# Kernel optimization log

Measured on AMD Instinct MI355X. Metric: run time of the kernel, lower is better.

The kernel has to match this reference:

```python
import math
import jax
import jax.numpy as jnp
import numpy as np

N_QUBITS = 4
N_LAYERS = 2


def _ry(t):
    # t: [] or [B] real angle -> [2,2] or [B,2,2] complex RY matrix
    c, s = jnp.cos(t * 0.5), jnp.sin(t * 0.5)
    return jnp.stack([jnp.stack([c, -s], -1), jnp.stack([s, c], -1)], -2).astype(jnp.complex64)


def _rz(t):
    # t: [] or [B] real angle -> diag(e^{-it/2}, e^{+it/2}) complex RZ matrix
    ph = jnp.exp(-0.5j * t.astype(jnp.complex64))
    z = jnp.zeros_like(ph)
    return jnp.stack([jnp.stack([ph, z], -1), jnp.stack([z, jnp.conj(ph)], -1)], -2)


def _apply_1q(psi, U, w):
    # psi: [B,2,2,2,2]; U: [2,2] (shared) or [B,2,2] (per-sample); wire w
    psi = jnp.moveaxis(psi, 1 + w, -1)
    if U.ndim == 3:
        out = jnp.einsum('bij,bpqrj->bpqri', U, psi)
    else:
        out = jnp.einsum('ij,bpqrj->bpqri', U, psi)
    return jnp.moveaxis(out, -1, 1 + w)


def _cnot(psi, c):
    # CNOT with control wire c, target wire c+1 (matches qml.CNOT([w, w+1]))
    a0 = jax.lax.index_in_dim(psi, 0, axis=1 + c, keepdims=False)
    a1 = jax.lax.index_in_dim(psi, 1, axis=1 + c, keepdims=False)
    a1 = jnp.flip(a1, axis=1 + c)
    return jnp.stack([a0, a1], axis=1 + c)


def _circuit(angles, q_weights):
    # angles: [B,4] real; q_weights: [n_layers,4,2]
    B = angles.shape[0]
    psi = jnp.zeros((B, 2, 2, 2, 2), jnp.complex64).at[:, 0, 0, 0, 0].set(1.0)
    for layer in range(N_LAYERS):
        for w in range(N_QUBITS):
            psi = _apply_1q(psi, _ry(angles[:, w]), w)
            psi = _apply_1q(psi, _rz((layer + 1) * angles[:, w]), w)
        for w in range(N_QUBITS):
            psi = _apply_1q(psi, _ry(q_weights[layer, w, 0]), w)
            psi = _apply_1q(psi, _rz(q_weights[layer, w, 1]), w)
        for w in range(N_QUBITS - 1):
            psi = _cnot(psi, w)
    p = psi.real ** 2 + psi.imag ** 2  # [B,2,2,2,2] probabilities
    zs = []
    for w in range(N_QUBITS):
        axes = tuple(a for a in range(1, 1 + N_QUBITS) if a != 1 + w)
        s = jnp.sum(p, axis=axes)  # [B,2]
        zs.append(s[:, 0] - s[:, 1])
    return jnp.stack(zs, -1).astype(jnp.float32)  # [B,4] <Z_w> expvals


def setup_inputs() -> dict:
    key = jax.random.key(0)
    ks = jax.random.split(key, 8)
    B, D = 131072, 256
    return {
        'x': jax.random.normal(ks[0], (B, D), jnp.float32),
        'w_proj': jax.random.normal(ks[1], (4, D), jnp.float32) / np.float32(np.sqrt(D)),
        'b_proj': jnp.zeros((4,), jnp.float32),
        'q_weights': 0.01 * jax.random.normal(ks[2], (2, 4, 2), jnp.float32),
        'w_h': jax.random.normal(ks[3], (16, 4), jnp.float32) * np.float32(0.5),
        'b_h': jnp.zeros((16,), jnp.float32),
        'w_out': jax.random.normal(ks[4], (10, 16), jnp.float32) * np.float32(0.25),
        'b_out': jnp.zeros((10,), jnp.float32),
    }


def reference(x, w_proj, b_proj, q_weights, w_h, b_h, w_out, b_out):
    # input_proj -> tanh * pi -> per-sample quantum circuit -> MLP classifier
    angles = jnp.tanh(x @ w_proj.T + b_proj) * np.float32(math.pi)  # [B,4]
    q = _circuit(angles, q_weights)                                  # [B,4]
    h = jax.nn.relu(q @ w_h.T + b_h)                                 # [B,16]
    return h @ w_out.T + b_out                                       # [B,10]
```

## Files before the change

### kernel.cpp

```cpp
#include <hip/hip_runtime.h>
#include <math.h>

#define D    256
#define BLK  64
#define RPC  8
#define NCH  (BLK/RPC)

struct C2 { float x, y; };

__device__ __forceinline__ float4 shfl_xor4(float4 a, int m) {
  float4 r;
  r.x = __shfl_xor(a.x, m); r.y = __shfl_xor(a.y, m);
  r.z = __shfl_xor(a.z, m); r.w = __shfl_xor(a.w, m);
  return r;
}
__device__ __forceinline__ float4 add4(float4 a, float4 b) {
  return make_float4(a.x+b.x, a.y+b.y, a.z+b.z, a.w+b.w);
}

__device__ __forceinline__ void gate_ry(C2 st[16], const int m, float c, float s) {
#pragma unroll
  for (int i = 0; i < 16; ++i) {
    if (i & m) continue;
    const int i1 = i | m;
    C2 a0 = st[i], a1 = st[i1];
    st[i].x  = c*a0.x - s*a1.x;  st[i].y  = c*a0.y - s*a1.y;
    st[i1].x = s*a0.x + c*a1.x;  st[i1].y = s*a0.y + c*a1.y;
  }
}

__device__ __forceinline__ void gate_rz(C2 st[16], const int m, float c, float s) {
#pragma unroll
  for (int i = 0; i < 16; ++i) {
    C2 a = st[i];
    if (i & m) { st[i].x = a.x*c - a.y*s; st[i].y = a.y*c + a.x*s; }
    else       { st[i].x = a.x*c + a.y*s; st[i].y = a.y*c - a.x*s; }
  }
}

__global__ __launch_bounds__(BLK, 4) void qhead_kernel(
    const float4* __restrict__ x4,
    const float*  __restrict__ w_proj,
    const float*  __restrict__ b_proj,
    const float*  __restrict__ qw,
    const float*  __restrict__ w_h,
    const float*  __restrict__ b_h,
    const float*  __restrict__ w_out,
    const float*  __restrict__ b_out,
    float*        __restrict__ out)
{
  __shared__ float outS[BLK * 11];

  const int tid = threadIdx.x;
  const long s0 = (long)blockIdx.x * BLK;
  const float4* xrow = x4 + s0 * (D / 4);

  float4 wj[4];
#pragma unroll
  for (int j = 0; j < 4; ++j)
    wj[j] = *(const float4*)(w_proj + j * D + 4 * tid);

  float4 v[8];
#pragma unroll
  for (int i = 0; i < 8; ++i) v[i] = xrow[(long)i * (D/4) + tid];

  const int b5 = (tid >> 5) & 1, b4 = (tid >> 4) & 1, b3 = (tid >> 3) & 1;
  const int csel = tid & 7;
  float4 acc = make_float4(0.f, 0.f, 0.f, 0.f);

#pragma unroll 1
  for (int c = 0; c < NCH; ++c) {
    float4 p[8];
#pragma unroll
    for (int i = 0; i < 8; ++i) {
      p[i].x = v[i].x*wj[0].x + v[i].y*wj[0].y + v[i].z*wj[0].z + v[i].w*wj[0].w;
      p[i].y = v[i].x*wj[1].x + v[i].y*wj[1].y + v[i].z*wj[1].z + v[i].w*wj[1].w;
      p[i].z = v[i].x*wj[2].x + v[i].y*wj[2].y + v[i].z*wj[2].z + v[i].w*wj[2].w;
      p[i].w = v[i].x*wj[3].x + v[i].y*wj[3].y + v[i].z*wj[3].z + v[i].w*wj[3].w;
    }
    if (c + 1 < NCH) {
#pragma unroll
      for (int i = 0; i < 8; ++i)
        v[i] = xrow[((long)(c + 1) * RPC + i) * (D/4) + tid];
    }
    float4 q[4];
#pragma unroll
    for (int i = 0; i < 4; ++i) {
      float4 send = b5 ? p[i] : p[i + 4];
      float4 keep = b5 ? p[i + 4] : p[i];
      q[i] = add4(keep, shfl_xor4(send, 32));
    }
    float4 u[2];
#pragma unroll
    for (int i = 0; i < 2; ++i) {
      float4 send = b4 ? u[0] : u[0];
      (void)send;
      float4 s2 = b4 ? q[i] : q[i + 2];
      float4 k2 = b4 ? q[i + 2] : q[i];
      u[i] = add4(k2, shfl_xor4(s2, 16));
    }
    float4 t;
    {
      float4 s3 = b3 ? u[0] : u[1];
      float4 k3 = b3 ? u[1] : u[0];
      t = add4(k3, shfl_xor4(s3, 8));
    }
    t = add4(t, shfl_xor4(t, 4));
    t = add4(t, shfl_xor4(t, 2));
    t = add4(t, shfl_xor4(t, 1));
    if (csel == c) acc = t;
  }

  const float PI_F = 3.14159265358979f;
  float ang[4];
  ang[0] = tanhf(acc.x + b_proj[0]) * PI_F;
  ang[1] = tanhf(acc.y + b_proj[1]) * PI_F;
  ang[2] = tanhf(acc.z + b_proj[2]) * PI_F;
  ang[3] = tanhf(acc.w + b_proj[3]) * PI_F;

  float ch[4], sh[4], cf[4], sf[4];
#pragma unroll
  for (int w = 0; w < 4; ++w) {
    __sincosf(0.5f * ang[w], &sh[w], &ch[w]);
    __sincosf(ang[w], &sf[w], &cf[w]);
  }

  C2 st[16];
#pragma unroll
  for (int i = 0; i < 16; ++i) { st[i].x = 0.f; st[i].y = 0.f; }
  st[0].x = 1.f;

#pragma unroll
  for (int layer = 0; layer < 2; ++layer) {
#pragma unroll
    for (int w = 0; w < 4; ++w) {
      gate_ry(st, 8 >> w, ch[w], sh[w]);
      if (layer == 0) gate_rz(st, 8 >> w, ch[w], sh[w]);
      else            gate_rz(st, 8 >> w, cf[w], sf[w]);
    }
#pragma unroll
    for (int w = 0; w < 4; ++w) {
      float cw, sw, cz, sz;
      __sincosf(0.5f * qw[(layer * 4 + w) * 2 + 0], &sw, &cw);
      __sincosf(0.5f * qw[(layer * 4 + w) * 2 + 1], &sz, &cz);
      gate_ry(st, 8 >> w, cw, sw);
      gate_rz(st, 8 >> w, cz, sz);
    }
#pragma unroll
    for (int w = 0; w < 3; ++w) {
      const int mc = 8 >> w, mt = 4 >> w;
#pragma unroll
      for (int i = 0; i < 16; ++i) {
        if ((i & mc) && !(i & mt)) {
          C2 t2 = st[i]; st[i] = st[i | mt]; st[i | mt] = t2;
        }
      }
    }
  }

  float z[4] = {0.f, 0.f, 0.f, 0.f};
#pragma unroll
  for (int i = 0; i < 16; ++i) {
    const float p = st[i].x * st[i].x + st[i].y * st[i].y;
#pragma unroll
    for (int w = 0; w < 4; ++w) z[w] += (i & (8 >> w)) ? -p : p;
  }

  float outv[10];
  {
    float h[16];
#pragma unroll
    for (int j = 0; j < 16; ++j) {
      float a = b_h[j];
#pragma unroll
      for (int w = 0; w < 4; ++w) a += w_h[j * 4 + w] * z[w];
      h[j] = fmaxf(a, 0.f);
    }
#pragma unroll
    for (int o = 0; o < 10; ++o) {
      float a = b_out[o];
#pragma unroll
      for (int j = 0; j < 16; ++j) a += w_out[o * 16 + j] * h[j];
      outv[o] = a;
    }
  }

  const int smp = 8 * csel + (tid >> 3);
#pragma unroll
  for (int o = 0; o < 10; ++o) outS[smp * 11 + o] = outv[o];
  __syncthreads();
  float* og = out + (long)blockIdx.x * (BLK * 10);
#pragma unroll
  for (int i = 0; i < 10; ++i) {
    const int j = i * BLK + tid;
    og[j] = outS[(j / 10) * 11 + (j % 10)];
  }
}

extern "C" void kernel_launch(void* const* d_in, const int* in_sizes, int n_in,
                              void* d_out, int out_size, void* d_ws, size_t ws_size,
                              hipStream_t stream) {
  const int B = in_sizes[0] / D;
  dim3 grid(B / BLK), block(BLK);
  qhead_kernel<<<grid, block, 0, stream>>>(
      (const float4*)d_in[0],
      (const float*)d_in[1], (const float*)d_in[2], (const float*)d_in[3],
      (const float*)d_in[4], (const float*)d_in[5], (const float*)d_in[6],
      (const float*)d_in[7], (float*)d_out);
}
```

Before: 210.8 us.

## Halve samples per block and double-buffer x row loads

Each block now handles 32 samples instead of 64, so the grid has twice as many blocks. Two register buffers of 8 rows each are kept, so loads for the next two chunks are in flight while the current chunk is reduced. The aim is more memory-level parallelism for what looks like a latency-bound projection. The cost is more registers (launch bounds lowered to 3) and every sample's circuit and MLP now being computed by two threads, which doubles that redundant compute.

```diff
diff --git a/kernel.cpp b/kernel.cpp
--- a/kernel.cpp
+++ b/kernel.cpp
@@ -3,8 +3,9 @@
 
 #define D    256
 #define BLK  64
+#define SPB  32
 #define RPC  8
-#define NCH  (BLK/RPC)
+#define NCH  (SPB/RPC)
 
 struct C2 { float x, y; };
 
@@ -38,7 +39,48 @@
   }
 }
 
-__global__ __launch_bounds__(BLK, 4) void qhead_kernel(
+#define PHASE(V, c)                                                          \
+  {                                                                          \
+    float4 p[8];                                                             \
+    _Pragma("unroll")                                                        \
+    for (int i = 0; i < 8; ++i) {                                            \
+      p[i].x = V[i].x*wj[0].x + V[i].y*wj[0].y + V[i].z*wj[0].z + V[i].w*wj[0].w; \
+      p[i].y = V[i].x*wj[1].x + V[i].y*wj[1].y + V[i].z*wj[1].z + V[i].w*wj[1].w; \
+      p[i].z = V[i].x*wj[2].x + V[i].y*wj[2].y + V[i].z*wj[2].z + V[i].w*wj[2].w; \
+      p[i].w = V[i].x*wj[3].x + V[i].y*wj[3].y + V[i].z*wj[3].z + V[i].w*wj[3].w; \
+    }                                                                        \
+    if ((c) + 2 < NCH) {                                                     \
+      _Pragma("unroll")                                                      \
+      for (int i = 0; i < 8; ++i)                                            \
+        V[i] = xrow[((long)((c) + 2) * RPC + i) * (D/4) + tid];              \
+    }                                                                        \
+    float4 q[4];                                                             \
+    _Pragma("unroll")                                                        \
+    for (int i = 0; i < 4; ++i) {                                            \
+      float4 snd = b5 ? p[i] : p[i + 4];                                     \
+      float4 kp  = b5 ? p[i + 4] : p[i];                                     \
+      q[i] = add4(kp, shfl_xor4(snd, 32));                                   \
+    }                                                                        \
+    float4 u[2];                                                             \
+    _Pragma("unroll")                                                        \
+    for (int i = 0; i < 2; ++i) {                                            \
+      float4 snd = b4 ? q[i] : q[i + 2];                                     \
+      float4 kp  = b4 ? q[i + 2] : q[i];                                     \
+      u[i] = add4(kp, shfl_xor4(snd, 16));                                   \
+    }                                                                        \
+    float4 t;                                                                \
+    {                                                                        \
+      float4 snd = b3 ? u[0] : u[1];                                         \
+      float4 kp  = b3 ? u[1] : u[0];                                         \
+      t = add4(kp, shfl_xor4(snd, 8));                                       \
+    }                                                                        \
+    t = add4(t, shfl_xor4(t, 4));                                            \
+    t = add4(t, shfl_xor4(t, 2));                                            \
+    t = add4(t, shfl_xor4(t, 1));                                            \
+    if (csel == (c)) acc = t;                                                \
+  }
+
+__global__ __launch_bounds__(BLK, 3) void qhead_kernel(
     const float4* __restrict__ x4,
     const float*  __restrict__ w_proj,
     const float*  __restrict__ b_proj,
@@ -49,10 +91,10 @@
     const float*  __restrict__ b_out,
     float*        __restrict__ out)
 {
-  __shared__ float outS[BLK * 11];
+  __shared__ float outS[SPB * 11];
 
   const int tid = threadIdx.x;
-  const long s0 = (long)blockIdx.x * BLK;
+  const long s0 = (long)blockIdx.x * SPB;
   const float4* xrow = x4 + s0 * (D / 4);
 
   float4 wj[4];
@@ -60,55 +102,20 @@
   for (int j = 0; j < 4; ++j)
     wj[j] = *(const float4*)(w_proj + j * D + 4 * tid);
 
-  float4 v[8];
-#pragma unroll
-  for (int i = 0; i < 8; ++i) v[i] = xrow[(long)i * (D/4) + tid];
-
   const int b5 = (tid >> 5) & 1, b4 = (tid >> 4) & 1, b3 = (tid >> 3) & 1;
-  const int csel = tid & 7;
+  const int csel = tid & 3;
   float4 acc = make_float4(0.f, 0.f, 0.f, 0.f);
 
+  float4 vA[8], vB[8];
+#pragma unroll
+  for (int i = 0; i < 8; ++i) vA[i] = xrow[(long)i * (D/4) + tid];
+#pragma unroll
+  for (int i = 0; i < 8; ++i) vB[i] = xrow[(long)(RPC + i) * (D/4) + tid];
+
 #pragma unroll 1
-  for (int c = 0; c < NCH; ++c) {
-    float4 p[8];
-#pragma unroll
-    for (int i = 0; i < 8; ++i) {
-      p[i].x = v[i].x*wj[0].x + v[i].y*wj[0].y + v[i].z*wj[0].z + v[i].w*wj[0].w;
-      p[i].y = v[i].x*wj[1].x + v[i].y*wj[1].y + v[i].z*wj[1].z + v[i].w*wj[1].w;
-      p[i].z = v[i].x*wj[2].x + v[i].y*wj[2].y + v[i].z*wj[2].z + v[i].w*wj[2].w;
-      p[i].w = v[i].x*wj[3].x + v[i].y*wj[3].y + v[i].z*wj[3].z + v[i].w*wj[3].w;
-    }
-    if (c + 1 < NCH) {
-#pragma unroll
-      for (int i = 0; i < 8; ++i)
-        v[i] = xrow[((long)(c + 1) * RPC + i) * (D/4) + tid];
-    }
-    float4 q[4];
-#pragma unroll
-    for (int i = 0; i < 4; ++i) {
-      float4 send = b5 ? p[i] : p[i + 4];
-      float4 keep = b5 ? p[i + 4] : p[i];
-      q[i] = add4(keep, shfl_xor4(send, 32));
-    }
-    float4 u[2];
-#pragma unroll
-    for (int i = 0; i < 2; ++i) {
-      float4 send = b4 ? u[0] : u[0];
-      (void)send;
-      float4 s2 = b4 ? q[i] : q[i + 2];
-      float4 k2 = b4 ? q[i + 2] : q[i];
-      u[i] = add4(k2, shfl_xor4(s2, 16));
-    }
-    float4 t;
-    {
-      float4 s3 = b3 ? u[0] : u[1];
-      float4 k3 = b3 ? u[1] : u[0];
-      t = add4(k3, shfl_xor4(s3, 8));
-    }
-    t = add4(t, shfl_xor4(t, 4));
-    t = add4(t, shfl_xor4(t, 2));
-    t = add4(t, shfl_xor4(t, 1));
-    if (csel == c) acc = t;
+  for (int cc = 0; cc < NCH; cc += 2) {
+    PHASE(vA, cc);
+    PHASE(vB, cc + 1);
   }
 
   const float PI_F = 3.14159265358979f;
@@ -189,9 +196,9 @@
 #pragma unroll
   for (int o = 0; o < 10; ++o) outS[smp * 11 + o] = outv[o];
   __syncthreads();
-  float* og = out + (long)blockIdx.x * (BLK * 10);
-#pragma unroll
-  for (int i = 0; i < 10; ++i) {
+  float* og = out + (long)blockIdx.x * (SPB * 10);
+#pragma unroll
+  for (int i = 0; i < 5; ++i) {
     const int j = i * BLK + tid;
     og[j] = outS[(j / 10) * 11 + (j % 10)];
   }
@@ -201,7 +208,7 @@
                               void* d_out, int out_size, void* d_ws, size_t ws_size,
                               hipStream_t stream) {
   const int B = in_sizes[0] / D;
-  dim3 grid(B / BLK), block(BLK);
+  dim3 grid(B / SPB), block(BLK);
   qhead_kernel<<<grid, block, 0, stream>>>(
       (const float4*)d_in[0],
       (const float*)d_in[1], (const float*)d_in[2], (const float*)d_in[3],
```

New measurement: 210.2 us. No clear change (-0.3%).
